# Kernel tuning notes

Hardware: AMD Instinct MI355X
Metric: run time of the kernel (lower is better)

Reference implementation:

```python
import jax, jax.numpy as jnp
import numpy as np

D_CONV = 4
D_STATE = 16
DT_RANK = 64


def _silu(x):
    return x * jax.nn.sigmoid(x)


def setup_inputs() -> dict:
    key = jax.random.key(0)
    ks = jax.random.split(key, 10)
    B, L, dim = 2, 1024, 1024
    d_inner = 2 * dim
    s = lambda fan: 1.0 / np.sqrt(fan)
    inp = {
        "x": jax.random.normal(ks[0], (B, L, dim), jnp.float32),
        "ln_w": jnp.ones((dim,), jnp.float32),
        "ln_b": jnp.zeros((dim,), jnp.float32),
        "w_in": jax.random.normal(ks[1], (2 * d_inner, dim), jnp.float32) * s(dim),
        "conv_w": jax.random.normal(ks[2], (d_inner, D_CONV), jnp.float32) * s(D_CONV),
        "conv_b": jnp.zeros((d_inner,), jnp.float32),
        "w_xproj": jax.random.normal(ks[3], (DT_RANK + 2 * D_STATE, d_inner), jnp.float32) * s(d_inner),
        "w_dt": jax.random.normal(ks[4], (d_inner, DT_RANK), jnp.float32) * s(DT_RANK),
        "b_dt": jax.random.normal(ks[5], (d_inner,), jnp.float32) * 0.1,
        # S4D-real init: A = -(1..d_state) per channel
        "a_log": jnp.tile(jnp.log(jnp.arange(1, D_STATE + 1, dtype=jnp.float32)), (d_inner, 1)),
        "d_skip": jnp.ones((d_inner,), jnp.float32),
        "w_out": jax.random.normal(ks[6], (dim, d_inner), jnp.float32) * s(d_inner),
    }
    return inp


def reference(x, ln_w, ln_b, w_in, conv_w, conv_b, w_xproj, w_dt, b_dt, a_log, d_skip, w_out):
    B, L, dim = x.shape
    residual = x

    # LayerNorm
    mu = jnp.mean(x, axis=-1, keepdims=True)
    var = jnp.mean((x - mu) ** 2, axis=-1, keepdims=True)
    xn = (x - mu) * jax.lax.rsqrt(var + 1e-5) * ln_w + ln_b

    # in_proj -> (x_ssm, z) each (B, L, d_inner)
    xz = jnp.einsum("bld,ed->ble", xn, w_in)
    d_inner = xz.shape[-1] // 2
    xs, z = xz[..., :d_inner], xz[..., d_inner:]

    # depthwise causal conv1d (kernel D_CONV) + SiLU
    xp = jnp.pad(xs, ((0, 0), (D_CONV - 1, 0), (0, 0)))
    xc = conv_b
    for k in range(D_CONV):
        xc = xc + conv_w[:, k] * xp[:, k : k + L, :]
    u = _silu(xc)  # (B, L, d_inner)

    # x_proj -> dt, B, C
    x_dbl = jnp.einsum("ble,re->blr", u, w_xproj)
    dt_r = x_dbl[..., :DT_RANK]
    B_ssm = x_dbl[..., DT_RANK : DT_RANK + D_STATE]         # (B, L, n)
    C_ssm = x_dbl[..., DT_RANK + D_STATE :]                 # (B, L, n)

    dt = jax.nn.softplus(jnp.einsum("blr,er->ble", dt_r, w_dt) + b_dt)  # (B, L, d_inner)

    A = -jnp.exp(a_log)  # (d_inner, n)
    deltaA = jnp.exp(jnp.einsum("ble,en->blen", dt, A))            # (B, L, e, n)
    deltaBu = jnp.einsum("ble,bln,ble->blen", dt, B_ssm, u)        # (B, L, e, n)

    # selective scan over L
    def step(h, ins):
        dA_t, dBu_t, C_t = ins
        h = dA_t * h + dBu_t                       # (B, e, n)
        y = jnp.einsum("ben,bn->be", h, C_t)
        return h, y

    h0 = jnp.zeros((B, d_inner, D_STATE), xs.dtype)
    _, ys = jax.lax.scan(
        step,
        h0,
        (deltaA.transpose(1, 0, 2, 3), deltaBu.transpose(1, 0, 2, 3), C_ssm.transpose(1, 0, 2)),
    )
    y = ys.transpose(1, 0, 2) + u * d_skip         # (B, L, e)

    y = y * _silu(z)
    out = jnp.einsum("ble,de->bld", y, w_out)
    return residual + out
```

## Files before the change

### kernel.cpp

```cpp
#include <hip/hip_runtime.h>
#include <hip/hip_bf16.h>


#define LC 16
#define NCHUNK 64

typedef short bf16x8 __attribute__((ext_vector_type(8)));
typedef float f32x4  __attribute__((ext_vector_type(4)));

static __device__ __forceinline__ float siluf(float x) { return x / (1.f + __expf(-x)); }
static __device__ __forceinline__ unsigned short f2bf(float f) {
    unsigned int u = __float_as_uint(f);
    unsigned int r = (u + 0x7fffu + ((u >> 16) & 1u)) >> 16;
    return (unsigned short)r;
}
static __device__ __forceinline__ float bfb(unsigned short u) {
    return __uint_as_float(((unsigned int)u) << 16);
}
static __device__ __forceinline__ void gload_lds16(const void* g, void* l) {
    __builtin_amdgcn_global_load_lds(
        (const __attribute__((address_space(1))) void*)g,
        (__attribute__((address_space(3))) void*)l, 16, 0, 0);
}

__global__ __launch_bounds__(256) void setup_kernel(
    const float* __restrict__ w_in,  unsigned short* __restrict__ w_in_b,
    const float* __restrict__ w_out, unsigned short* __restrict__ w_out_b,
    const float* __restrict__ w_dt,  unsigned short* __restrict__ w_dt_b,
    const float* __restrict__ x,
    const float* __restrict__ ln_w,
    const float* __restrict__ ln_b,
    unsigned short* __restrict__ xn)
{
    int bid = blockIdx.x, tid = threadIdx.x;
    if (bid < 6272) {
        int i = bid * 256 + tid;
        const float* in; unsigned short* outp; int j;
        if (i < 1048576)      { in = w_in;  outp = w_in_b;  j = i; }
        else if (i < 1572864) { in = w_out; outp = w_out_b; j = i - 1048576; }
        else if (i < 1605632) { in = w_dt;  outp = w_dt_b;  j = i - 1572864; }
        else return;
        float4 v = reinterpret_cast<const float4*>(in)[j];
        ushort4 o = { f2bf(v.x), f2bf(v.y), f2bf(v.z), f2bf(v.w) };
        reinterpret_cast<ushort4*>(outp)[j] = o;
        return;
    }
    int m = bid - 6272;
    const float4* xr = reinterpret_cast<const float4*>(x) + (size_t)m * 256;
    float4 r = xr[tid];
    float f0 = r.x, f1 = r.y, f2 = r.z, f3 = r.w;
    float s  = f0 + f1 + f2 + f3;
    float s2 = f0*f0 + f1*f1 + f2*f2 + f3*f3;
    #pragma unroll
    for (int off = 32; off > 0; off >>= 1) {
        s  += __shfl_down(s, off);
        s2 += __shfl_down(s2, off);
    }
    __shared__ float red[8];
    if ((tid & 63) == 0) { red[tid >> 6] = s; red[4 + (tid >> 6)] = s2; }
    __syncthreads();
    float st = red[0] + red[1] + red[2] + red[3];
    float qt = red[4] + red[5] + red[6] + red[7];
    float mu   = st * (1.f / 1024.f);
    float var  = qt * (1.f / 1024.f) - mu * mu;
    float rstd = rsqrtf(var + 1e-5f);
    float4 wv = reinterpret_cast<const float4*>(ln_w)[tid];
    float4 bv = reinterpret_cast<const float4*>(ln_b)[tid];
    ushort4 o = { f2bf((f0 - mu) * rstd * wv.x + bv.x),
                  f2bf((f1 - mu) * rstd * wv.y + bv.y),
                  f2bf((f2 - mu) * rstd * wv.z + bv.z),
                  f2bf((f3 - mu) * rstd * wv.w + bv.w) };
    reinterpret_cast<ushort4*>(xn + (size_t)m * 1024)[tid] = o;
}

__global__ __launch_bounds__(256) void gemm_bf16_nt(
    const unsigned short* __restrict__ A, int lda,
    const unsigned short* __restrict__ B, int ldb,
    int Kslice,
    float* __restrict__ C, unsigned short* __restrict__ Cb, int ldc,
    int ep, size_t Cstride)
{
    __shared__ short As[3 * 64 * 32];
    __shared__ short Bs[3 * 128 * 32];
    int tid = threadIdx.x;
    int z = blockIdx.z;
    A += (size_t)z * Kslice;
    B += (size_t)z * Kslice;
    C += (size_t)z * Cstride;

    int gx = gridDim.x;
    int wg = blockIdx.y * gx + blockIdx.x;
    int nwg = gx * gridDim.y;
    int cpx = nwg >> 3;
    int swz = (wg & 7) * cpx + (wg >> 3);
    int bx = swz % gx, by = swz / gx;

    int m0 = by * 64, n0 = bx * 128;
    int lane = tid & 63, wave = tid >> 6;
    int wm = (wave >> 1) * 32, wn = (wave & 1) * 64;
    int frow = lane & 15, fq = lane >> 4;

    f32x4 acc[2][4] = {};

    int lrow = lane >> 2;
    int scol = (lane & 3) * 8;
    const unsigned short* AgL = A + (size_t)(m0 + wave * 16 + lrow) * lda + scol;
    const unsigned short* BgL = B + (size_t)(n0 + wave * 16 + lrow) * ldb + scol;
    int aoff = (wave * 16) * 32;
    int boff = (wave * 16) * 32;

    #pragma unroll
    for (int p = 0; p < 2; ++p) {
        int nk = p * 32;
        gload_lds16(AgL + nk,                    As + p * 2048 + aoff);
        gload_lds16(BgL + nk,                    Bs + p * 4096 + boff);
        gload_lds16(BgL + (size_t)64 * ldb + nk, Bs + p * 4096 + boff + 64 * 32);
    }

    int cur = 0;
    for (int k0 = 0; k0 < Kslice; k0 += 32) {
        if (k0 + 32 < Kslice) {
            asm volatile("s_waitcnt vmcnt(3) lgkmcnt(0)" ::: "memory");
        } else {
            asm volatile("s_waitcnt vmcnt(0) lgkmcnt(0)" ::: "memory");
        }
        __builtin_amdgcn_s_barrier();
        int nk = k0 + 64;
        if (nk < Kslice) {
            int stg = cur - 1; if (stg < 0) stg = 2;
            gload_lds16(AgL + nk,                    As + stg * 2048 + aoff);
            gload_lds16(BgL + nk,                    Bs + stg * 4096 + boff);
            gload_lds16(BgL + (size_t)64 * ldb + nk, Bs + stg * 4096 + boff + 64 * 32);
        }
        const short* Ac = As + cur * 2048;
        const short* Bc = Bs + cur * 4096;
        bf16x8 af[2], bfr[4];
        #pragma unroll
        for (int i = 0; i < 2; ++i)
            af[i] = *reinterpret_cast<const bf16x8*>(Ac + (wm + i * 16 + frow) * 32 + fq * 8);
        #pragma unroll
        for (int j = 0; j < 4; ++j)
            bfr[j] = *reinterpret_cast<const bf16x8*>(Bc + (wn + j * 16 + frow) * 32 + fq * 8);
        #pragma unroll
        for (int i = 0; i < 2; ++i)
            #pragma unroll
            for (int j = 0; j < 4; ++j)
                acc[i][j] = __builtin_amdgcn_mfma_f32_16x16x32_bf16(af[i], bfr[j], acc[i][j], 0, 0, 0);
        cur = (cur == 2) ? 0 : cur + 1;
    }

    int cn = lane & 15, rq = (lane >> 4) * 4;
    #pragma unroll
    for (int i = 0; i < 2; ++i) {
        #pragma unroll
        for (int j = 0; j < 4; ++j) {
            #pragma unroll
            for (int r = 0; r < 4; ++r) {
                int row = m0 + wm + i * 16 + rq + r;
                int col = n0 + wn + j * 16 + cn;
                float v = acc[i][j][r];
                if (ep == 0) {
                    C[(size_t)row * ldc + col] = v;
                } else {
                    Cb[(size_t)row * ldc + col] = f2bf(v);
                }
            }
        }
    }
}

__global__ __launch_bounds__(256) void out_reduce(
    const float* __restrict__ part, const float* __restrict__ x,
    float* __restrict__ out)
{
    int i = blockIdx.x * 256 + threadIdx.x;
    float4 s = reinterpret_cast<const float4*>(x)[i];
    #pragma unroll
    for (int z = 0; z < 4; ++z) {
        float4 p = reinterpret_cast<const float4*>(part + (size_t)z * 2097152)[i];
        s.x += p.x; s.y += p.y; s.z += p.z; s.w += p.w;
    }
    reinterpret_cast<float4*>(out)[i] = s;
}

__global__ __launch_bounds__(256) void xproj_splitk(
    const unsigned short* __restrict__ xz,
    const float* __restrict__ cw,
    const float* __restrict__ cb,
    const float* __restrict__ B,
    unsigned short* __restrict__ u,
    float* __restrict__ part)
{
    __shared__ float As[16][68];
    __shared__ float Bs[16][100];
    int tid = threadIdx.x;
    int m0 = blockIdx.x * 64;
    int k0 = blockIdx.y * 64;
    int tx = tid & 15;
    int ty = tid >> 4;
    float acc[4][6] = {};
    int arow = tid >> 2, akg = (tid & 3) << 2;
    int brow1 = (256 + tid) >> 2, bkg1 = ((256 + tid) & 3) << 2;
    int m = m0 + arow;
    int l = m & 1023;

    for (int ks = 0; ks < 64; ks += 16) {
        int e0 = k0 + ks + akg;
        float xv[4][4];
        #pragma unroll
        for (int kk = 0; kk < 4; ++kk) {
            ushort4 t = make_ushort4(0, 0, 0, 0);
            if (l - 3 + kk >= 0)
                t = *reinterpret_cast<const ushort4*>(xz + (size_t)(m - 3 + kk) * 4096 + e0);
            xv[kk][0] = bfb(t.x); xv[kk][1] = bfb(t.y);
            xv[kk][2] = bfb(t.z); xv[kk][3] = bfb(t.w);
        }
        float4 cbv = *reinterpret_cast<const float4*>(cb + e0);
        float cbs[4] = { cbv.x, cbv.y, cbv.z, cbv.w };
        float res[4];
        #pragma unroll
        for (int j = 0; j < 4; ++j) {
            float4 w = *reinterpret_cast<const float4*>(cw + (size_t)(e0 + j) * 4);
            float a = cbs[j];
            a = fmaf(w.x, xv[0][j], a);
            a = fmaf(w.y, xv[1][j], a);
            a = fmaf(w.z, xv[2][j], a);
            a = fmaf(w.w, xv[3][j], a);
            res[j] = siluf(a);
        }
        ushort4 uo = { f2bf(res[0]), f2bf(res[1]), f2bf(res[2]), f2bf(res[3]) };
        *reinterpret_cast<ushort4*>(u + (size_t)m * 2048 + e0) = uo;

        float4 bv0 = make_float4(0.f, 0.f, 0.f, 0.f), bv1 = bv0;
        if (arow < 96)  bv0 = *reinterpret_cast<const float4*>(B + (size_t)arow * 2048 + k0 + ks + akg);
        if (brow1 < 96) bv1 = *reinterpret_cast<const float4*>(B + (size_t)brow1 * 2048 + k0 + ks + bkg1);
        __syncthreads();
        As[akg + 0][arow] = res[0]; As[akg + 1][arow] = res[1];
        As[akg + 2][arow] = res[2]; As[akg + 3][arow] = res[3];
        if (arow < 96) {
            Bs[akg + 0][arow] = bv0.x; Bs[akg + 1][arow] = bv0.y;
            Bs[akg + 2][arow] = bv0.z; Bs[akg + 3][arow] = bv0.w;
        }
        if (brow1 < 96) {
            Bs[bkg1 + 0][brow1] = bv1.x; Bs[bkg1 + 1][brow1] = bv1.y;
            Bs[bkg1 + 2][brow1] = bv1.z; Bs[bkg1 + 3][brow1] = bv1.w;
        }
        __syncthreads();
        #pragma unroll
        for (int k = 0; k < 16; ++k) {
            float aa[4], bb[6];
            #pragma unroll
            for (int i = 0; i < 4; ++i) aa[i] = As[k][ty * 4 + i];
            #pragma unroll
            for (int j = 0; j < 6; ++j) bb[j] = Bs[k][tx * 6 + j];
            #pragma unroll
            for (int i = 0; i < 4; ++i)
                #pragma unroll
                for (int j = 0; j < 6; ++j)
                    acc[i][j] = fmaf(aa[i], bb[j], acc[i][j]);
        }
    }
    float* p = part + (size_t)blockIdx.y * 196608;
    #pragma unroll
    for (int i = 0; i < 4; ++i)
        #pragma unroll
        for (int j = 0; j < 6; ++j)
            p[(size_t)(m0 + ty * 4 + i) * 96 + tx * 6 + j] = acc[i][j];
}

__global__ __launch_bounds__(256) void xproj_reduce(
    const float* __restrict__ part, float* __restrict__ xdbl)
{
    int i = blockIdx.x * 256 + threadIdx.x;
    float s = 0.f;
    #pragma unroll
    for (int sd = 0; sd < 32; ++sd) s += part[(size_t)sd * 196608 + i];
    xdbl[i] = s;
}

static __device__ __forceinline__ void dt_tile16(
    const float* __restrict__ xdbl, const unsigned short* __restrict__ w_dt_b,
    const float* __restrict__ b_dt, size_t rbase, int et,
    int lane, int wave, float dtl[LC][128])
{
    int frow = lane & 15, fq = lane >> 4;
    bf16x8 af[2];
    #pragma unroll
    for (int kk = 0; kk < 2; ++kk) {
        const float* ap = xdbl + (rbase + frow) * 96 + kk * 32 + fq * 8;
        float4 a0 = *reinterpret_cast<const float4*>(ap);
        float4 a1 = *reinterpret_cast<const float4*>(ap + 4);
        bf16x8 t;
        t[0] = (short)f2bf(a0.x); t[1] = (short)f2bf(a0.y);
        t[2] = (short)f2bf(a0.z); t[3] = (short)f2bf(a0.w);
        t[4] = (short)f2bf(a1.x); t[5] = (short)f2bf(a1.y);
        t[6] = (short)f2bf(a1.z); t[7] = (short)f2bf(a1.w);
        af[kk] = t;
    }
    f32x4 dacc[2] = {};
    #pragma unroll
    for (int j = 0; j < 2; ++j)
        #pragma unroll
        for (int kk = 0; kk < 2; ++kk) {
            int row_e = et * 128 + wave * 32 + j * 16 + frow;
            bf16x8 bfr = *reinterpret_cast<const bf16x8*>(
                w_dt_b + (size_t)row_e * 64 + kk * 32 + fq * 8);
            dacc[j] = __builtin_amdgcn_mfma_f32_16x16x32_bf16(af[kk], bfr, dacc[j], 0, 0, 0);
        }
    int cn = lane & 15, rq = (lane >> 4) * 4;
    #pragma unroll
    for (int j = 0; j < 2; ++j)
        #pragma unroll
        for (int r = 0; r < 4; ++r) {
            int row = rq + r;
            int col = wave * 32 + j * 16 + cn;
            float v = dacc[j][r] + b_dt[et * 128 + col];
            float ex = __expf(v);
            v = (v > 20.f) ? v : __logf(1.f + ex);
            dtl[row][col] = bfb(f2bf(v));
        }
}

__global__ __launch_bounds__(256) void scan_part1(
    const unsigned short* __restrict__ u,
    const float* __restrict__ xdbl,
    const unsigned short* __restrict__ w_dt_b,
    const float* __restrict__ b_dt,
    const float* __restrict__ a_log,
    float* __restrict__ hpart,
    float* __restrict__ Aprod)
{
    __shared__ float dtl[LC][128];
    __shared__ float Bl[LC][16];
    __shared__ unsigned short ul[LC][128];
    int tid = threadIdx.x;
    int lane = tid & 63, wave = tid >> 6;
    int bid = blockIdx.x;
    int c = bid & 63, et = (bid >> 6) & 15, b = bid >> 10;
    int ch = tid >> 1, ng = tid & 1;
    int e = et * 128 + ch;
    size_t rbase = (size_t)b * 1024 + c * LC;

    {
        int r = tid >> 4, o = (tid & 15) * 8;
        *reinterpret_cast<float4*>(&ul[r][o]) =
            *reinterpret_cast<const float4*>(u + (rbase + r) * 2048 + et * 128 + o);
    }
    Bl[tid >> 4][tid & 15] = xdbl[(rbase + (tid >> 4)) * 96 + 64 + (tid & 15)];

    dt_tile16(xdbl, w_dt_b, b_dt, rbase, et, lane, wave, dtl);

    float A[8];
    {
        float4 a0 = *reinterpret_cast<const float4*>(a_log + (size_t)e * 16 + ng * 8);
        float4 a1 = *reinterpret_cast<const float4*>(a_log + (size_t)e * 16 + ng * 8 + 4);
        A[0] = -__expf(a0.x); A[1] = -__expf(a0.y);
        A[2] = -__expf(a0.z); A[3] = -__expf(a0.w);
        A[4] = -__expf(a1.x); A[5] = -__expf(a1.y);
        A[6] = -__expf(a1.z); A[7] = -__expf(a1.w);
    }
    float h[8];
    #pragma unroll
    for (int n = 0; n < 8; ++n) h[n] = 0.f;
    float S = 0.f;

    __syncthreads();
    #pragma unroll
    for (int l = 0; l < LC; ++l) {
        float dtv = dtl[l][ch];
        float u_c = bfb(ul[l][ch]);
        float4 b0 = *reinterpret_cast<const float4*>(&Bl[l][ng * 8]);
        float4 b1 = *reinterpret_cast<const float4*>(&Bl[l][ng * 8 + 4]);
        float Bv[8] = { b0.x, b0.y, b0.z, b0.w, b1.x, b1.y, b1.z, b1.w };
        float du = dtv * u_c;
        S += dtv;
        #pragma unroll
        for (int n = 0; n < 8; ++n) {
            float d = __expf(dtv * A[n]);
            h[n] = fmaf(d, h[n], du * Bv[n]);
        }
    }
    float P[8];
    #pragma unroll
    for (int n = 0; n < 8; ++n) P[n] = __expf(A[n] * S);

    size_t oidx = (size_t)c * 65536 + ((size_t)b * 2048 + e) * 16 + ng * 8;
    *reinterpret_cast<float4*>(hpart + oidx)     = make_float4(h[0], h[1], h[2], h[3]);
    *reinterpret_cast<float4*>(hpart + oidx + 4) = make_float4(h[4], h[5], h[6], h[7]);
    *reinterpret_cast<float4*>(Aprod + oidx)     = make_float4(P[0], P[1], P[2], P[3]);
    *reinterpret_cast<float4*>(Aprod + oidx + 4) = make_float4(P[4], P[5], P[6], P[7]);
}

__global__ __launch_bounds__(256) void scan_combine(
    const float* __restrict__ hpart,
    const float* __restrict__ Aprod,
    float* __restrict__ hinit)
{
    int t = blockIdx.x * 256 + threadIdx.x;
    float h = 0.f;
    #pragma unroll 8
    for (int c = 0; c < NCHUNK; ++c) {
        hinit[(size_t)c * 65536 + t] = h;
        float P  = Aprod[(size_t)c * 65536 + t];
        float hp = hpart[(size_t)c * 65536 + t];
        h = fmaf(P, h, hp);
    }
}

__global__ __launch_bounds__(256) void scan_part2(
    const unsigned short* __restrict__ u,
    const float* __restrict__ xdbl,
    const unsigned short* __restrict__ w_dt_b,
    const float* __restrict__ b_dt,
    const unsigned short* __restrict__ xz,
    const float* __restrict__ a_log,
    const float* __restrict__ d_skip,
    const float* __restrict__ hinit,
    unsigned short* __restrict__ y)
{
    __shared__ float dtl[LC][128];
    __shared__ float BCl[LC][32];
    __shared__ unsigned short ul[LC][128];
    __shared__ unsigned short zl[LC][128];
    int tid = threadIdx.x;
    int lane = tid & 63, wave = tid >> 6;
    int bid = blockIdx.x;
    int c = bid & 63, et = (bid >> 6) & 15, b = bid >> 10;
    int ch = tid >> 1, ng = tid & 1;
    int e = et * 128 + ch;
    size_t rbase = (size_t)b * 1024 + c * LC;

    {
        int r = tid >> 4, o = (tid & 15) * 8;
        *reinterpret_cast<float4*>(&ul[r][o]) =
            *reinterpret_cast<const float4*>(u + (rbase + r) * 2048 + et * 128 + o);
        *reinterpret_cast<float4*>(&zl[r][o]) =
            *reinterpret_cast<const float4*>(xz + (rbase + r) * 4096 + 2048 + et * 128 + o);
    }
    #pragma unroll
    for (int s = 0; s < 2; ++s) {
        int idx = s * 256 + tid;
        BCl[idx >> 5][idx & 31] = xdbl[(rbase + (idx >> 5)) * 96 + 64 + (idx & 31)];
    }

    dt_tile16(xdbl, w_dt_b, b_dt, rbase, et, lane, wave, dtl);

    float A[8];
    {
        float4 a0 = *reinterpret_cast<const float4*>(a_log + (size_t)e * 16 + ng * 8);
        float4 a1 = *reinterpret_cast<const float4*>(a_log + (size_t)e * 16 + ng * 8 + 4);
        A[0] = -__expf(a0.x); A[1] = -__expf(a0.y);
        A[2] = -__expf(a0.z); A[3] = -__expf(a0.w);
        A[4] = -__expf(a1.x); A[5] = -__expf(a1.y);
        A[6] = -__expf(a1.z); A[7] = -__expf(a1.w);
    }
    float dsk = d_skip[e];
    float h[8];
    size_t oidx = (size_t)c * 65536 + ((size_t)b * 2048 + e) * 16 + ng * 8;
    {
        float4 h0 = *reinterpret_cast<const float4*>(hinit + oidx);
        float4 h1 = *reinterpret_cast<const float4*>(hinit + oidx + 4);
        h[0] = h0.x; h[1] = h0.y; h[2] = h0.z; h[3] = h0.w;
        h[4] = h1.x; h[5] = h1.y; h[6] = h1.z; h[7] = h1.w;
    }

    unsigned short* y_p = y + rbase * 2048 + e;
    __syncthreads();
    #pragma unroll
    for (int l = 0; l < LC; ++l) {
        float dtv = dtl[l][ch];
        float u_c = bfb(ul[l][ch]);
        float4 b0 = *reinterpret_cast<const float4*>(&BCl[l][ng * 8]);
        float4 b1 = *reinterpret_cast<const float4*>(&BCl[l][ng * 8 + 4]);
        float4 c0 = *reinterpret_cast<const float4*>(&BCl[l][16 + ng * 8]);
        float4 c1 = *reinterpret_cast<const float4*>(&BCl[l][16 + ng * 8 + 4]);
        float Bv[8] = { b0.x, b0.y, b0.z, b0.w, b1.x, b1.y, b1.z, b1.w };
        float Cv[8] = { c0.x, c0.y, c0.z, c0.w, c1.x, c1.y, c1.z, c1.w };
        float du = dtv * u_c;
        float p = 0.f;
        #pragma unroll
        for (int n = 0; n < 8; ++n) {
            float d = __expf(dtv * A[n]);
            h[n] = fmaf(d, h[n], du * Bv[n]);
            p = fmaf(h[n], Cv[n], p);
        }
        p += __shfl_xor(p, 1);
        if (ng == 0) {
            float zv = bfb(zl[l][ch]);
            y_p[(size_t)l * 2048] = f2bf((p + u_c * dsk) * siluf(zv));
        }
    }
}

extern "C" void kernel_launch(void* const* d_in, const int* in_sizes, int n_in,
                              void* d_out, int out_size, void* d_ws, size_t ws_size,
                              hipStream_t stream) {
    const float* x       = (const float*)d_in[0];
    const float* ln_w    = (const float*)d_in[1];
    const float* ln_b    = (const float*)d_in[2];
    const float* w_in    = (const float*)d_in[3];
    const float* conv_w  = (const float*)d_in[4];
    const float* conv_b  = (const float*)d_in[5];
    const float* w_xproj = (const float*)d_in[6];
    const float* w_dt    = (const float*)d_in[7];
    const float* b_dt    = (const float*)d_in[8];
    const float* a_log   = (const float*)d_in[9];
    const float* d_skip  = (const float*)d_in[10];
    const float* w_out   = (const float*)d_in[11];
    float* out = (float*)d_out;

    float* ws = (float*)d_ws;
    unsigned short* xn_b    = (unsigned short*)(ws);
    unsigned short* xz_b    = (unsigned short*)(ws + 1048576);
    unsigned short* u_b     = (unsigned short*)(ws + 5242880);
    float* xdbl  = ws + 7340032;
    float* hpart = ws + 9633792;
    float* Aprod = ws + 13828096;
    float* hinit = ws + 18022400;
    unsigned short* y_b     = (unsigned short*)(ws + 22216704);
    unsigned short* w_in_b  = (unsigned short*)(ws + 24313856);
    unsigned short* w_out_b = (unsigned short*)(ws + 26411008);
    unsigned short* w_dt_b  = (unsigned short*)(ws + 27459584);
    float* xpart = ws + 9633792;
    float* opart = ws + 1048576;

    setup_kernel<<<8320, 256, 0, stream>>>(w_in, w_in_b, w_out, w_out_b, w_dt, w_dt_b,
                                           x, ln_w, ln_b, xn_b);
    gemm_bf16_nt<<<dim3(32, 32, 1), 256, 0, stream>>>(xn_b, 1024, w_in_b, 1024, 1024,
                                                      nullptr, xz_b, 4096, 3, 0);
    xproj_splitk<<<dim3(32, 32), 256, 0, stream>>>(xz_b, conv_w, conv_b, w_xproj,
                                                   u_b, xpart);
    xproj_reduce<<<768, 256, 0, stream>>>(xpart, xdbl);
    scan_part1<<<2048, 256, 0, stream>>>(u_b, xdbl, w_dt_b, b_dt, a_log, hpart, Aprod);
    scan_combine<<<256, 256, 0, stream>>>(hpart, Aprod, hinit);
    scan_part2<<<2048, 256, 0, stream>>>(u_b, xdbl, w_dt_b, b_dt, xz_b, a_log,
                                         d_skip, hinit, y_b);
    gemm_bf16_nt<<<dim3(8, 32, 4), 256, 0, stream>>>(y_b, 2048, w_out_b, 2048, 512,
                                                     opart, nullptr, 1024, 0, 2097152);
    out_reduce<<<2048, 256, 0, stream>>>(opart, x, out);
}
```

Measured before the change: 237.5 us.

## Double scan chunk length and stage scan output through LDS for coalesced stores

The selective-scan chunk length goes from 16 to 32 timesteps, which halves the chunk count and the grid size of both scan passes. The dt projection tile is widened to compute 32 rows with MFMA, reusing each w_dt fragment across two row tiles. scan_part2 now writes its gated outputs into the shared z buffer and then stores y as 16-byte vectors, replacing scattered 2-byte global stores. The trade-off is a longer serial recurrence per block, fewer blocks to hide latency, and an extra block barrier.

```diff
diff --git a/kernel.cpp b/kernel.cpp
--- a/kernel.cpp
+++ b/kernel.cpp
@@ -2,8 +2,8 @@
 #include <hip/hip_bf16.h>
 
 
-#define LC 16
-#define NCHUNK 64
+#define LC 32
+#define NCHUNK 32
 
 typedef short bf16x8 __attribute__((ext_vector_type(8)));
 typedef float f32x4  __attribute__((ext_vector_type(4)));
@@ -278,26 +278,28 @@
     xdbl[i] = s;
 }
 
-static __device__ __forceinline__ void dt_tile16(
+static __device__ __forceinline__ void dt_tile32(
     const float* __restrict__ xdbl, const unsigned short* __restrict__ w_dt_b,
     const float* __restrict__ b_dt, size_t rbase, int et,
     int lane, int wave, float dtl[LC][128])
 {
     int frow = lane & 15, fq = lane >> 4;
-    bf16x8 af[2];
-    #pragma unroll
-    for (int kk = 0; kk < 2; ++kk) {
-        const float* ap = xdbl + (rbase + frow) * 96 + kk * 32 + fq * 8;
-        float4 a0 = *reinterpret_cast<const float4*>(ap);
-        float4 a1 = *reinterpret_cast<const float4*>(ap + 4);
-        bf16x8 t;
-        t[0] = (short)f2bf(a0.x); t[1] = (short)f2bf(a0.y);
-        t[2] = (short)f2bf(a0.z); t[3] = (short)f2bf(a0.w);
-        t[4] = (short)f2bf(a1.x); t[5] = (short)f2bf(a1.y);
-        t[6] = (short)f2bf(a1.z); t[7] = (short)f2bf(a1.w);
-        af[kk] = t;
-    }
-    f32x4 dacc[2] = {};
+    bf16x8 af[2][2];
+    #pragma unroll
+    for (int i = 0; i < 2; ++i)
+        #pragma unroll
+        for (int kk = 0; kk < 2; ++kk) {
+            const float* ap = xdbl + (rbase + i * 16 + frow) * 96 + kk * 32 + fq * 8;
+            float4 a0 = *reinterpret_cast<const float4*>(ap);
+            float4 a1 = *reinterpret_cast<const float4*>(ap + 4);
+            bf16x8 t;
+            t[0] = (short)f2bf(a0.x); t[1] = (short)f2bf(a0.y);
+            t[2] = (short)f2bf(a0.z); t[3] = (short)f2bf(a0.w);
+            t[4] = (short)f2bf(a1.x); t[5] = (short)f2bf(a1.y);
+            t[6] = (short)f2bf(a1.z); t[7] = (short)f2bf(a1.w);
+            af[i][kk] = t;
+        }
+    f32x4 dacc[2][2] = {};
     #pragma unroll
     for (int j = 0; j < 2; ++j)
         #pragma unroll
@@ -305,20 +307,24 @@
             int row_e = et * 128 + wave * 32 + j * 16 + frow;
             bf16x8 bfr = *reinterpret_cast<const bf16x8*>(
                 w_dt_b + (size_t)row_e * 64 + kk * 32 + fq * 8);
-            dacc[j] = __builtin_amdgcn_mfma_f32_16x16x32_bf16(af[kk], bfr, dacc[j], 0, 0, 0);
+            #pragma unroll
+            for (int i = 0; i < 2; ++i)
+                dacc[i][j] = __builtin_amdgcn_mfma_f32_16x16x32_bf16(af[i][kk], bfr, dacc[i][j], 0, 0, 0);
         }
     int cn = lane & 15, rq = (lane >> 4) * 4;
     #pragma unroll
-    for (int j = 0; j < 2; ++j)
-        #pragma unroll
-        for (int r = 0; r < 4; ++r) {
-            int row = rq + r;
-            int col = wave * 32 + j * 16 + cn;
-            float v = dacc[j][r] + b_dt[et * 128 + col];
-            float ex = __expf(v);
-            v = (v > 20.f) ? v : __logf(1.f + ex);
-            dtl[row][col] = bfb(f2bf(v));
-        }
+    for (int i = 0; i < 2; ++i)
+        #pragma unroll
+        for (int j = 0; j < 2; ++j)
+            #pragma unroll
+            for (int r = 0; r < 4; ++r) {
+                int row = i * 16 + rq + r;
+                int col = wave * 32 + j * 16 + cn;
+                float v = dacc[i][j][r] + b_dt[et * 128 + col];
+                float ex = __expf(v);
+                v = (v > 20.f) ? v : __logf(1.f + ex);
+                dtl[row][col] = bfb(f2bf(v));
+            }
 }
 
 __global__ __launch_bounds__(256) void scan_part1(
@@ -336,19 +342,25 @@
     int tid = threadIdx.x;
     int lane = tid & 63, wave = tid >> 6;
     int bid = blockIdx.x;
-    int c = bid & 63, et = (bid >> 6) & 15, b = bid >> 10;
+    int c = bid & 31, et = (bid >> 5) & 15, b = bid >> 9;
     int ch = tid >> 1, ng = tid & 1;
     int e = et * 128 + ch;
     size_t rbase = (size_t)b * 1024 + c * LC;
 
-    {
-        int r = tid >> 4, o = (tid & 15) * 8;
+    #pragma unroll
+    for (int s = 0; s < 2; ++s) {
+        int idx = s * 256 + tid;
+        int r = idx >> 4, o = (idx & 15) * 8;
         *reinterpret_cast<float4*>(&ul[r][o]) =
             *reinterpret_cast<const float4*>(u + (rbase + r) * 2048 + et * 128 + o);
     }
-    Bl[tid >> 4][tid & 15] = xdbl[(rbase + (tid >> 4)) * 96 + 64 + (tid & 15)];
-
-    dt_tile16(xdbl, w_dt_b, b_dt, rbase, et, lane, wave, dtl);
+    #pragma unroll
+    for (int s = 0; s < 2; ++s) {
+        int idx = s * 256 + tid;
+        Bl[idx >> 4][idx & 15] = xdbl[(rbase + (idx >> 4)) * 96 + 64 + (idx & 15)];
+    }
+
+    dt_tile32(xdbl, w_dt_b, b_dt, rbase, et, lane, wave, dtl);
 
     float A[8];
     {
@@ -425,25 +437,27 @@
     int tid = threadIdx.x;
     int lane = tid & 63, wave = tid >> 6;
     int bid = blockIdx.x;
-    int c = bid & 63, et = (bid >> 6) & 15, b = bid >> 10;
+    int c = bid & 31, et = (bid >> 5) & 15, b = bid >> 9;
     int ch = tid >> 1, ng = tid & 1;
     int e = et * 128 + ch;
     size_t rbase = (size_t)b * 1024 + c * LC;
 
-    {
-        int r = tid >> 4, o = (tid & 15) * 8;
+    #pragma unroll
+    for (int s = 0; s < 2; ++s) {
+        int idx = s * 256 + tid;
+        int r = idx >> 4, o = (idx & 15) * 8;
         *reinterpret_cast<float4*>(&ul[r][o]) =
             *reinterpret_cast<const float4*>(u + (rbase + r) * 2048 + et * 128 + o);
         *reinterpret_cast<float4*>(&zl[r][o]) =
             *reinterpret_cast<const float4*>(xz + (rbase + r) * 4096 + 2048 + et * 128 + o);
     }
     #pragma unroll
-    for (int s = 0; s < 2; ++s) {
+    for (int s = 0; s < 4; ++s) {
         int idx = s * 256 + tid;
         BCl[idx >> 5][idx & 31] = xdbl[(rbase + (idx >> 5)) * 96 + 64 + (idx & 31)];
     }
 
-    dt_tile16(xdbl, w_dt_b, b_dt, rbase, et, lane, wave, dtl);
+    dt_tile32(xdbl, w_dt_b, b_dt, rbase, et, lane, wave, dtl);
 
     float A[8];
     {
@@ -464,7 +478,6 @@
         h[4] = h1.x; h[5] = h1.y; h[6] = h1.z; h[7] = h1.w;
     }
 
-    unsigned short* y_p = y + rbase * 2048 + e;
     __syncthreads();
     #pragma unroll
     for (int l = 0; l < LC; ++l) {
@@ -487,8 +500,16 @@
         p += __shfl_xor(p, 1);
         if (ng == 0) {
             float zv = bfb(zl[l][ch]);
-            y_p[(size_t)l * 2048] = f2bf((p + u_c * dsk) * siluf(zv));
-        }
+            zl[l][ch] = f2bf((p + u_c * dsk) * siluf(zv));
+        }
+    }
+    __syncthreads();
+    #pragma unroll
+    for (int s = 0; s < 2; ++s) {
+        int idx = s * 256 + tid;
+        int r = idx >> 4, o = (idx & 15) * 8;
+        *reinterpret_cast<float4*>(y + (rbase + r) * 2048 + et * 128 + o) =
+            *reinterpret_cast<const float4*>(&zl[r][o]);
     }
 }
 
@@ -531,9 +552,9 @@
     xproj_splitk<<<dim3(32, 32), 256, 0, stream>>>(xz_b, conv_w, conv_b, w_xproj,
                                                    u_b, xpart);
     xproj_reduce<<<768, 256, 0, stream>>>(xpart, xdbl);
-    scan_part1<<<2048, 256, 0, stream>>>(u_b, xdbl, w_dt_b, b_dt, a_log, hpart, Aprod);
+    scan_part1<<<1024, 256, 0, stream>>>(u_b, xdbl, w_dt_b, b_dt, a_log, hpart, Aprod);
     scan_combine<<<256, 256, 0, stream>>>(hpart, Aprod, hinit);
-    scan_part2<<<2048, 256, 0, stream>>>(u_b, xdbl, w_dt_b, b_dt, xz_b, a_log,
+    scan_part2<<<1024, 256, 0, stream>>>(u_b, xdbl, w_dt_b, b_dt, xz_b, a_log,
                                          d_skip, hinit, y_b);
     gemm_bf16_nt<<<dim3(8, 32, 4), 256, 0, stream>>>(y_b, 2048, w_out_b, 2048, 512,
                                                      opart, nullptr, 1024, 0, 2097152);
```

After: 238.0 us. No clear change (+0.2%).
